# Optimization experiments

Hardware: AMD Instinct MI355X
Metric: run time of the kernel (lower is better)

The kernel has to match this reference:

```python
import jax, jax.numpy as jnp
import numpy as np

NUM_HEADS = 8
LN_EPS = 1e-5


def _layernorm(x, g, b):
    m = jnp.mean(x, axis=-1, keepdims=True)
    v = jnp.mean(jnp.square(x - m), axis=-1, keepdims=True)
    return (x - m) * jax.lax.rsqrt(v + LN_EPS) * g + b


def setup_inputs() -> dict:
    key = jax.random.key(0)
    ks = jax.random.split(key, 10)
    D, C, Cin = 2, 256, 64  # depth, embed dim, input channels
    w = lambda k, shape: jax.random.normal(k, shape, jnp.float32) * 0.02
    return {
        "x": jax.random.normal(ks[0], (4, Cin, 12, 12, 12), jnp.float32),
        "W_pe": w(ks[1], (Cin, C)),
        "b_pe": jnp.zeros((C,), jnp.float32),
        "cls_token": w(ks[2], (1, 1, C)),
        "ln1_g": jnp.ones((D, C), jnp.float32),
        "ln1_b": jnp.zeros((D, C), jnp.float32),
        "Wqkv": w(ks[3], (D, C, 3 * C)),
        "Wproj": w(ks[4], (D, C, C)),
        "bproj": jnp.zeros((D, C), jnp.float32),
        "ln2_g": jnp.ones((D, C), jnp.float32),
        "ln2_b": jnp.zeros((D, C), jnp.float32),
        "W1": w(ks[5], (D, C, C)),
        "b1": jnp.zeros((D, C), jnp.float32),
        "W2": w(ks[6], (D, C, C)),
        "b2": jnp.zeros((D, C), jnp.float32),
        "normf_g": jnp.ones((C,), jnp.float32),
        "normf_b": jnp.zeros((C,), jnp.float32),
    }


def reference(x, W_pe, b_pe, cls_token, ln1_g, ln1_b, Wqkv, Wproj, bproj,
              ln2_g, ln2_b, W1, b1, W2, b2, normf_g, normf_b):
    B, Cin, H, W, L = x.shape
    C = W_pe.shape[1]
    hd = C // NUM_HEADS
    scale = hd ** (-0.5)

    # PatchEmbed: 1x1x1 Conv3d == per-voxel linear projection, then flatten to tokens
    tok = jnp.einsum('bchwl,cd->bhwld', x, W_pe).reshape(B, H * W * L, C) + b_pe
    cls = jnp.broadcast_to(cls_token, (B, 1, C))
    t = jnp.concatenate([cls, tok], axis=1)  # [B, N, C], N = H*W*L + 1
    N = t.shape[1]

    depth = Wqkv.shape[0]
    for i in range(depth):
        # --- self-attention ---
        y = _layernorm(t, ln1_g[i], ln1_b[i])
        qkv = (y @ Wqkv[i]).reshape(B, N, 3, NUM_HEADS, hd)
        qkv = jnp.transpose(qkv, (2, 0, 3, 1, 4))  # [3, B, H, N, hd]
        q, k, v = qkv[0], qkv[1], qkv[2]
        attn = jnp.einsum('bhnd,bhmd->bhnm', q, k) * scale
        attn = jax.nn.softmax(attn, axis=-1)
        o = jnp.einsum('bhnm,bhmd->bhnd', attn, v)
        o = jnp.transpose(o, (0, 2, 1, 3)).reshape(B, N, C)
        t = t + (o @ Wproj[i] + bproj[i])
        # --- MLP (mlp_ratio=1.0, exact GELU) ---
        y = _layernorm(t, ln2_g[i], ln2_b[i])
        h = jax.nn.gelu(y @ W1[i] + b1[i], approximate=False)
        t = t + (h @ W2[i] + b2[i])

    t = _layernorm(t, normf_g, normf_b)
    x_cls = t[:, 0]                                   # [B, C]
    feat = t[:, 1:]                                   # [B, H*W*L, C]
    feat = jnp.transpose(feat, (0, 2, 1)).reshape(B, C, H, W, L)  # downsample = Identity for dim=256
    return x_cls, feat
```

## Files before the change

kernel.cpp:

```cpp
#include <hip/hip_runtime.h>
#include <hip/hip_bf16.h>
#include <math.h>

#define B_   4
#define CIN  64
#define P_   1728
#define N_   1729
#define C_   256
#define NH_  8
#define HD_  32
#define M_   (B_*N_)
#define NPAD 1792

typedef __bf16 bf16x8 __attribute__((ext_vector_type(8)));
typedef __bf16 bf16x4 __attribute__((ext_vector_type(4)));
typedef float  f32x4  __attribute__((ext_vector_type(4)));
typedef float  f32x16 __attribute__((ext_vector_type(16)));

__global__ __launch_bounds__(256) void embed2(
    const float* __restrict__ x, const float* __restrict__ Wpe,
    const float* __restrict__ bpe, const float* __restrict__ cls,
    float* __restrict__ t)
{
    int idx = blockIdx.x*256 + threadIdx.x;
    int c   = idx & 255;
    int n   = (idx >> 8) % N_;
    int b   = idx / (N_*256);
    if (n == 0) { t[idx] = cls[c]; return; }
    int p = n - 1;
    float acc = bpe[c];
    for (int ci = 0; ci < CIN; ++ci)
        acc += x[(size_t)(b*CIN + ci)*P_ + p] * Wpe[ci*C_ + c];
    t[idx] = acc;
}

__global__ __launch_bounds__(256) void ln4(
    const float* __restrict__ in, __bf16* __restrict__ out,
    const float* __restrict__ g, const float* __restrict__ bb)
{
    int wv = threadIdx.x >> 6, lane = threadIdx.x & 63;
    size_t row = (size_t)blockIdx.x*4 + wv;
    float4 v = *(const float4*)&in[row*C_ + lane*4];
    float s1 = (v.x+v.y)+(v.z+v.w);
    float s2 = (v.x*v.x+v.y*v.y)+(v.z*v.z+v.w*v.w);
    #pragma unroll
    for (int off = 32; off >= 1; off >>= 1) {
        s1 += __shfl_xor(s1, off);
        s2 += __shfl_xor(s2, off);
    }
    float mean = s1*(1.0f/C_);
    float var  = fmaxf(s2*(1.0f/C_) - mean*mean, 0.0f);
    float rstd = rsqrtf(var + 1e-5f);
    float4 gg = *(const float4*)&g[lane*4];
    float4 bv = *(const float4*)&bb[lane*4];
    bf16x4 r;
    r[0] = (__bf16)((v.x-mean)*rstd*gg.x + bv.x);
    r[1] = (__bf16)((v.y-mean)*rstd*gg.y + bv.y);
    r[2] = (__bf16)((v.z-mean)*rstd*gg.z + bv.z);
    r[3] = (__bf16)((v.w-mean)*rstd*gg.w + bv.w);
    *(bf16x4*)&out[row*C_ + lane*4] = r;
}

__global__ __launch_bounds__(256) void ln4f(
    const float* __restrict__ in, float* __restrict__ out,
    const float* __restrict__ g, const float* __restrict__ bb,
    float* __restrict__ cls_out)
{
    int wv = threadIdx.x >> 6, lane = threadIdx.x & 63;
    size_t row = (size_t)blockIdx.x*4 + wv;
    float4 v = *(const float4*)&in[row*C_ + lane*4];
    float s1 = (v.x+v.y)+(v.z+v.w);
    float s2 = (v.x*v.x+v.y*v.y)+(v.z*v.z+v.w*v.w);
    #pragma unroll
    for (int off = 32; off >= 1; off >>= 1) {
        s1 += __shfl_xor(s1, off);
        s2 += __shfl_xor(s2, off);
    }
    float mean = s1*(1.0f/C_);
    float var  = fmaxf(s2*(1.0f/C_) - mean*mean, 0.0f);
    float rstd = rsqrtf(var + 1e-5f);
    float4 gg = *(const float4*)&g[lane*4];
    float4 bv = *(const float4*)&bb[lane*4];
    float4 r;
    r.x = (v.x-mean)*rstd*gg.x + bv.x;
    r.y = (v.y-mean)*rstd*gg.y + bv.y;
    r.z = (v.z-mean)*rstd*gg.z + bv.z;
    r.w = (v.w-mean)*rstd*gg.w + bv.w;
    *(float4*)&out[row*C_ + lane*4] = r;
    if ((row % N_) == 0)
        *(float4*)&cls_out[(row / N_)*C_ + lane*4] = r;
}

__global__ __launch_bounds__(256) void wprep2(
    const float* __restrict__ Wqkv, const float* __restrict__ Wproj,
    const float* __restrict__ W1,   const float* __restrict__ W2,
    __bf16* __restrict__ wT)
{
    int z = blockIdx.z, which = z >> 1, layer = z & 1;
    const float* src; __bf16* dst; int NC;
    if (which == 0) {
        src = Wqkv + (size_t)layer*C_*768;
        dst = wT   + (size_t)layer*768*256;
        NC  = 768;
    } else {
        NC = 256;
        const float* b3 = (which == 1) ? Wproj : (which == 2) ? W1 : W2;
        src = b3 + (size_t)layer*65536;
        dst = wT + 2*768*256 + (size_t)((which-1)*2 + layer)*65536;
    }
    int n0 = blockIdx.x*32; if (n0 >= NC) return;
    int k0 = blockIdx.y*32;
    __shared__ float tile[32][33];
    int c = threadIdx.x & 31, r = threadIdx.x >> 5;
    for (int rr = r; rr < 32; rr += 8)
        tile[rr][c] = src[(size_t)(k0+rr)*NC + n0 + c];
    __syncthreads();
    for (int rr = r; rr < 32; rr += 8)
        dst[(size_t)(n0+rr)*256 + k0 + c] = (__bf16)tile[c][rr];
}

__global__ __launch_bounds__(256) void padzero(
    __bf16* __restrict__ kB, __bf16* __restrict__ vB)
{
    int idx = blockIdx.x*256 + threadIdx.x;
    if (idx >= 32*63*32) return;
    int d  = idx & 31;
    int n  = (idx >> 5) % 63 + N_;
    int bh = idx / (63*32);
    kB[((size_t)bh*NPAD + n)*32 + d] = (__bf16)0.f;
    vB[((size_t)bh*32 + d)*NPAD + n] = (__bf16)0.f;
}

template<int NC, bool ADD, bool GELU, bool BIAS, bool OUTBF>
__global__ __launch_bounds__(256) void gemm3(
    const __bf16* __restrict__ A, const __bf16* __restrict__ Wt,
    const float* __restrict__ bias, float* __restrict__ outF,
    __bf16* __restrict__ outB)
{
    __shared__ __align__(16) __bf16 As[64*64];
    __shared__ __align__(16) __bf16 Bs[64*64];
    int r0 = blockIdx.x*64, c0 = blockIdx.y*64;
    int tid = threadIdx.x;
    int wv = tid >> 6, lane = tid & 63, quad = lane >> 4, mn = lane & 15;
    int sr = tid >> 2, sc = tid & 3;
    int ga = r0 + sr; if (ga >= M_) ga = M_ - 1;

    f32x4 acc[4];
    #pragma unroll
    for (int ct = 0; ct < 4; ++ct)
        #pragma unroll
        for (int rr = 0; rr < 4; ++rr) acc[ct][rr] = 0.f;

    for (int kc = 0; kc < 4; ++kc) {
        __syncthreads();
        *(bf16x8*)&As[sr*64 + ((sc ^ (sr & 7))*8)] =
            *(const bf16x8*)&A[(size_t)ga*256 + kc*64 + sc*8];
        *(bf16x8*)&As[sr*64 + (((sc+4) ^ (sr & 7))*8)] =
            *(const bf16x8*)&A[(size_t)ga*256 + kc*64 + sc*8 + 32];
        *(bf16x8*)&Bs[sr*64 + ((sc ^ (sr & 7))*8)] =
            *(const bf16x8*)&Wt[(size_t)(c0+sr)*256 + kc*64 + sc*8];
        *(bf16x8*)&Bs[sr*64 + (((sc+4) ^ (sr & 7))*8)] =
            *(const bf16x8*)&Wt[(size_t)(c0+sr)*256 + kc*64 + sc*8 + 32];
        __syncthreads();

        #pragma unroll
        for (int h = 0; h < 2; ++h) {
            bf16x8 a = *(const bf16x8*)&As[(wv*16 + mn)*64 + (((h*4+quad) ^ (mn & 7))*8)];
            #pragma unroll
            for (int ct = 0; ct < 4; ++ct) {
                bf16x8 b = *(const bf16x8*)&Bs[(ct*16 + mn)*64 + (((h*4+quad) ^ (mn & 7))*8)];
                acc[ct] = __builtin_amdgcn_mfma_f32_16x16x32_bf16(a, b, acc[ct], 0, 0, 0);
            }
        }
    }

    #pragma unroll
    for (int ct = 0; ct < 4; ++ct) {
        int col = c0 + ct*16 + mn;
        #pragma unroll
        for (int rr = 0; rr < 4; ++rr) {
            int row = r0 + wv*16 + quad*4 + rr;
            if (row >= M_) continue;
            float val = acc[ct][rr];
            if (BIAS) val += bias[col];
            if (GELU) val = 0.5f*val*(1.f + erff(val*0.70710678118654752f));
            size_t oi = (size_t)row*NC + col;
            if (OUTBF) outB[oi] = (__bf16)val;
            else if (ADD) outF[oi] += val;
            else outF[oi] = val;
        }
    }
}

__global__ __launch_bounds__(256) void gemm_qkv3(
    const __bf16* __restrict__ A, const __bf16* __restrict__ Wt,
    __bf16* __restrict__ qB, __bf16* __restrict__ kB, __bf16* __restrict__ vB)
{
    __shared__ __align__(16) __bf16 As[64*64];
    __shared__ __align__(16) __bf16 Bs[64*64];
    int r0 = blockIdx.x*64, c0 = blockIdx.y*64;
    int tid = threadIdx.x;
    int wv = tid >> 6, lane = tid & 63, quad = lane >> 4, mn = lane & 15;
    int sr = tid >> 2, sc = tid & 3;
    int ga = r0 + sr; if (ga >= M_) ga = M_ - 1;

    f32x4 acc[4];
    #pragma unroll
    for (int ct = 0; ct < 4; ++ct)
        #pragma unroll
        for (int rr = 0; rr < 4; ++rr) acc[ct][rr] = 0.f;

    for (int kc = 0; kc < 4; ++kc) {
        __syncthreads();
        *(bf16x8*)&As[sr*64 + ((sc ^ (sr & 7))*8)] =
            *(const bf16x8*)&A[(size_t)ga*256 + kc*64 + sc*8];
        *(bf16x8*)&As[sr*64 + (((sc+4) ^ (sr & 7))*8)] =
            *(const bf16x8*)&A[(size_t)ga*256 + kc*64 + sc*8 + 32];
        *(bf16x8*)&Bs[sr*64 + ((sc ^ (sr & 7))*8)] =
            *(const bf16x8*)&Wt[(size_t)(c0+sr)*256 + kc*64 + sc*8];
        *(bf16x8*)&Bs[sr*64 + (((sc+4) ^ (sr & 7))*8)] =
            *(const bf16x8*)&Wt[(size_t)(c0+sr)*256 + kc*64 + sc*8 + 32];
        __syncthreads();

        #pragma unroll
        for (int h = 0; h < 2; ++h) {
            bf16x8 a = *(const bf16x8*)&As[(wv*16 + mn)*64 + (((h*4+quad) ^ (mn & 7))*8)];
            #pragma unroll
            for (int ct = 0; ct < 4; ++ct) {
                bf16x8 b = *(const bf16x8*)&Bs[(ct*16 + mn)*64 + (((h*4+quad) ^ (mn & 7))*8)];
                acc[ct] = __builtin_amdgcn_mfma_f32_16x16x32_bf16(a, b, acc[ct], 0, 0, 0);
            }
        }
    }

    const float scale = 0.17677669529663687f;
    #pragma unroll
    for (int ct = 0; ct < 4; ++ct) {
        int col = c0 + ct*16 + mn;
        #pragma unroll
        for (int rr = 0; rr < 4; ++rr) {
            int row = r0 + wv*16 + quad*4 + rr;
            if (row >= M_) continue;
            int b = row / N_, n = row - b*N_;
            float val = acc[ct][rr];
            if (col < 256) {
                int h = col >> 5, dd = col & 31;
                qB[((size_t)(b*NH_+h)*NPAD + n)*32 + dd] = (__bf16)(val*scale);
            } else if (col < 512) {
                int h = (col-256) >> 5, dd = col & 31;
                kB[((size_t)(b*NH_+h)*NPAD + n)*32 + dd] = (__bf16)val;
            } else {
                int h = (col-512) >> 5, dd = col & 31;
                vB[((size_t)(b*NH_+h)*32 + dd)*NPAD + n] = (__bf16)val;
            }
        }
    }
}

#define LKS 40
#define LVS 136

__device__ __forceinline__ unsigned cvtpk_bf16(float lo, float hi) {
    unsigned r;
    asm("v_cvt_pk_bf16_f32 %0, %1, %2" : "=v"(r) : "v"(lo), "v"(hi));
    return r;
}

__global__ __launch_bounds__(128) void attn12(
    const __bf16* __restrict__ qB, const __bf16* __restrict__ kB,
    const __bf16* __restrict__ vB, __bf16* __restrict__ o)
{
    int bh = blockIdx.x, b = bh >> 3, h = bh & 7;
    int q0 = blockIdx.y * 64;
    int tid = threadIdx.x;
    int wv = tid >> 6, lane = tid & 63, lo5 = lane & 31, hi = lane >> 5;

    __shared__ __align__(16) __bf16 lk[128*LKS];
    __shared__ __align__(16) __bf16 lvt[32*LVS];

    const __bf16* kbase = kB + (size_t)bh*NPAD*32;
    const __bf16* vbase = vB + (size_t)bh*32*NPAD;

    const __bf16* qrow = qB + ((size_t)bh*NPAD + q0 + wv*32 + lo5)*32 + hi*8;
    bf16x8 qf0 = *(const bf16x8*)(qrow);
    bf16x8 qf1 = *(const bf16x8*)(qrow + 16);

    f32x16 oacc;
    #pragma unroll
    for (int r = 0; r < 16; ++r) oacc[r] = 0.f;
    float lsum = 0.f;

    int vr = tid >> 2, vc = tid & 3;

    bf16x8 ks0, ks1, ks2, ks3, vs0, vs1, vs2, vs3;
#define ATTN_LOAD(T) do {                                              \
        const __bf16* kp_ = kbase + ((size_t)((T)*128 + tid))*32;      \
        ks0 = *(const bf16x8*)(kp_);                                   \
        ks1 = *(const bf16x8*)(kp_ + 8);                               \
        ks2 = *(const bf16x8*)(kp_ + 16);                              \
        ks3 = *(const bf16x8*)(kp_ + 24);                              \
        const __bf16* vp_ = vbase + (size_t)vr*NPAD + (T)*128 + vc*32; \
        vs0 = *(const bf16x8*)(vp_);                                   \
        vs1 = *(const bf16x8*)(vp_ + 8);                               \
        vs2 = *(const bf16x8*)(vp_ + 16);                              \
        vs3 = *(const bf16x8*)(vp_ + 24);                              \
    } while (0)

    ATTN_LOAD(0);

    for (int t = 0; t < 14; ++t) {
        __syncthreads();
        {
            __bf16* kd = &lk[tid*LKS];
            *(bf16x8*)(kd)      = ks0;  *(bf16x8*)(kd + 8)  = ks1;
            *(bf16x8*)(kd + 16) = ks2;  *(bf16x8*)(kd + 24) = ks3;
            __bf16* vd = &lvt[vr*LVS + vc*32];
            *(bf16x8*)(vd)      = vs0;  *(bf16x8*)(vd + 8)  = vs1;
            *(bf16x8*)(vd + 16) = vs2;  *(bf16x8*)(vd + 24) = vs3;
        }
        if (t < 13) ATTN_LOAD(t+1);
        __syncthreads();

        #pragma unroll
        for (int kg = 0; kg < 4; ++kg) {
            const __bf16* kf = &lk[(kg*32 + lo5)*LKS + hi*8];
            bf16x8 kf0 = *(const bf16x8*)(kf);
            bf16x8 kf1 = *(const bf16x8*)(kf + 16);
            f32x16 s;
            #pragma unroll
            for (int r = 0; r < 16; ++r) s[r] = 0.f;
            __builtin_amdgcn_s_setprio(1);
            s = __builtin_amdgcn_mfma_f32_32x32x16_bf16(kf0, qf0, s, 0, 0, 0);
            s = __builtin_amdgcn_mfma_f32_32x32x16_bf16(kf1, qf1, s, 0, 0, 0);
            __builtin_amdgcn_s_setprio(0);

            float p[16];
            #pragma unroll
            for (int r = 0; r < 16; ++r) p[r] = __expf(s[r]);
            float l0 = 0.f, l1 = 0.f;
            #pragma unroll
            for (int r = 0; r < 8; ++r) { l0 += p[r]; l1 += p[r+8]; }
            lsum += l0 + l1;

            unsigned a0 = cvtpk_bf16(p[0],  p[1]),  a1 = cvtpk_bf16(p[2],  p[3]);
            unsigned b0 = cvtpk_bf16(p[4],  p[5]),  b1 = cvtpk_bf16(p[6],  p[7]);
            unsigned c0 = cvtpk_bf16(p[8],  p[9]),  c1 = cvtpk_bf16(p[10], p[11]);
            unsigned d0 = cvtpk_bf16(p[12], p[13]), d1 = cvtpk_bf16(p[14], p[15]);
            asm("v_permlane32_swap_b32 %0, %1" : "+v"(a0), "+v"(b0));
            asm("v_permlane32_swap_b32 %0, %1" : "+v"(a1), "+v"(b1));
            asm("v_permlane32_swap_b32 %0, %1" : "+v"(c0), "+v"(d0));
            asm("v_permlane32_swap_b32 %0, %1" : "+v"(c1), "+v"(d1));
            union { bf16x8 v; unsigned u[4]; } f0, f1;
            f0.u[0] = a0; f0.u[1] = a1; f0.u[2] = b0; f0.u[3] = b1;
            f1.u[0] = c0; f1.u[1] = c1; f1.u[2] = d0; f1.u[3] = d1;

            const __bf16* vf = &lvt[lo5*LVS + kg*32 + hi*8];
            bf16x8 vf0 = *(const bf16x8*)(vf);
            bf16x8 vf1 = *(const bf16x8*)(vf + 16);
            __builtin_amdgcn_s_setprio(1);
            oacc = __builtin_amdgcn_mfma_f32_32x32x16_bf16(f0.v, vf0, oacc, 0, 0, 0);
            oacc = __builtin_amdgcn_mfma_f32_32x32x16_bf16(f1.v, vf1, oacc, 0, 0, 0);
            __builtin_amdgcn_s_setprio(0);
        }
    }
#undef ATTN_LOAD

    lsum += __shfl_xor(lsum, 32);
    float inv = 1.0f / (lsum - 63.0f);

    #pragma unroll
    for (int r = 0; r < 16; ++r) {
        int qrw = (r & 3) + 8*(r >> 2) + 4*hi;
        float li = __shfl(inv, qrw);
        int q = q0 + wv*32 + qrw;
        if (q < N_)
            o[((size_t)b*N_ + q)*C_ + h*HD_ + lo5] = (__bf16)(oacc[r] * li);
    }
}

__global__ __launch_bounds__(256) void feat3(
    const float* __restrict__ y, float* __restrict__ outf)
{
    __shared__ float tl[32][33];
    int p0 = blockIdx.x*32, c0 = blockIdx.y*32, b = blockIdx.z;
    int cc = threadIdx.x & 31, rr = threadIdx.x >> 5;
    for (int i = rr; i < 32; i += 8)
        tl[i][cc] = y[((size_t)(b*N_) + 1 + p0 + i)*C_ + c0 + cc];
    __syncthreads();
    for (int i = rr; i < 32; i += 8)
        outf[((size_t)(b*C_) + c0 + i)*P_ + p0 + cc] = tl[cc][i];
}

extern "C" void kernel_launch(void* const* d_in, const int* in_sizes, int n_in,
                              void* d_out, int out_size, void* d_ws, size_t ws_size,
                              hipStream_t stream)
{
    const float* x        = (const float*)d_in[0];
    const float* W_pe     = (const float*)d_in[1];
    const float* b_pe     = (const float*)d_in[2];
    const float* cls_tok  = (const float*)d_in[3];
    const float* ln1_g    = (const float*)d_in[4];
    const float* ln1_b    = (const float*)d_in[5];
    const float* Wqkv     = (const float*)d_in[6];
    const float* Wproj    = (const float*)d_in[7];
    const float* bproj    = (const float*)d_in[8];
    const float* ln2_g    = (const float*)d_in[9];
    const float* ln2_b    = (const float*)d_in[10];
    const float* W1       = (const float*)d_in[11];
    const float* b1       = (const float*)d_in[12];
    const float* W2       = (const float*)d_in[13];
    const float* b2       = (const float*)d_in[14];
    const float* normf_g  = (const float*)d_in[15];
    const float* normf_b  = (const float*)d_in[16];

    const size_t MC = (size_t)M_*C_;
    float*  ws  = (float*)d_ws;
    float*  t   = ws;
    float*  yf  = ws + MC;
    __bf16* ybf = (__bf16*)(ws + 2*MC);
    __bf16* hbf = (__bf16*)(ws + 2*MC + MC/2);
    __bf16* obf = (__bf16*)(ws + 2*MC + MC);
    __bf16* wT  = (__bf16*)(ws + 2*MC + 3*(MC/2));
    __bf16* qB  = wT + 2*768*256 + 6*256*256;
    __bf16* kB  = qB + (size_t)B_*NH_*NPAD*32;
    __bf16* vB  = kB + (size_t)B_*NH_*NPAD*32;

    __bf16* projT = wT + 2*768*256;
    __bf16* w1T   = projT + 2*256*256;
    __bf16* w2T   = w1T   + 2*256*256;

    float* out_cls  = (float*)d_out;
    float* out_feat = out_cls + B_*C_;

    wprep2<<<dim3(24, 8, 8), 256, 0, stream>>>(Wqkv, Wproj, W1, W2, wT);
    padzero<<<252, 256, 0, stream>>>(kB, vB);
    embed2<<<(B_*N_*C_)/256, 256, 0, stream>>>(x, W_pe, b_pe, cls_tok, t);

    const int GRID_M = (M_ + 63) / 64;
    for (int i = 0; i < 2; ++i) {
        ln4<<<M_/4, 256, 0, stream>>>(t, ybf, ln1_g + i*C_, ln1_b + i*C_);
        gemm_qkv3<<<dim3(GRID_M, 12), 256, 0, stream>>>(
            ybf, wT + (size_t)i*768*256, qB, kB, vB);
        attn12<<<dim3(32, 28), 128, 0, stream>>>(qB, kB, vB, obf);
        gemm3<256,true,false,true,false><<<dim3(GRID_M, 4), 256, 0, stream>>>(
            obf, projT + (size_t)i*65536, bproj + i*C_, t, nullptr);
        ln4<<<M_/4, 256, 0, stream>>>(t, ybf, ln2_g + i*C_, ln2_b + i*C_);
        gemm3<256,false,true,true,true><<<dim3(GRID_M, 4), 256, 0, stream>>>(
            ybf, w1T + (size_t)i*65536, b1 + i*C_, nullptr, hbf);
        gemm3<256,true,false,true,false><<<dim3(GRID_M, 4), 256, 0, stream>>>(
            hbf, w2T + (size_t)i*65536, b2 + i*C_, t, nullptr);
    }

    ln4f<<<M_/4, 256, 0, stream>>>(t, yf, normf_g, normf_b, out_cls);
    feat3<<<dim3(54, 8, 4), 256, 0, stream>>>(yf, out_feat);
}
```

Baseline: 289.5 us.

## Double-buffer LDS tiles in GEMMs and attention, use exp2 with folded scale

Gives the GEMM kernels and the attention kernel two LDS buffers, so the next K/V or A/B tile is loaded from global and stored into the spare buffer while MFMAs run on the current one. This halves the barriers per iteration. Attention also issues all four QK^T MFMA groups before the softmax, splits the PV accumulation across two accumulators to shorten the dependency chain, and swaps __expf for raw v_exp_f32 with log2(e) folded into the q scale. The cost is doubled LDS usage and more live registers, which may reduce occupancy.

Result: no change. 288.7 us (-0.3%).

```diff
diff --git a/kernel.cpp b/kernel.cpp
--- a/kernel.cpp
+++ b/kernel.cpp
@@ -132,13 +132,13 @@
 }
 
 template<int NC, bool ADD, bool GELU, bool BIAS, bool OUTBF>
-__global__ __launch_bounds__(256) void gemm3(
+__global__ __launch_bounds__(256) void gemm4(
     const __bf16* __restrict__ A, const __bf16* __restrict__ Wt,
     const float* __restrict__ bias, float* __restrict__ outF,
     __bf16* __restrict__ outB)
 {
-    __shared__ __align__(16) __bf16 As[64*64];
-    __shared__ __align__(16) __bf16 Bs[64*64];
+    __shared__ __align__(16) __bf16 As[2][64*64];
+    __shared__ __align__(16) __bf16 Bs[2][64*64];
     int r0 = blockIdx.x*64, c0 = blockIdx.y*64;
     int tid = threadIdx.x;
     int wv = tid >> 6, lane = tid & 63, quad = lane >> 4, mn = lane & 15;
@@ -151,28 +151,46 @@
         #pragma unroll
         for (int rr = 0; rr < 4; ++rr) acc[ct][rr] = 0.f;
 
+    bf16x8 ra0, ra1, rb0, rb1;
+#define GLOAD(KC) do {                                                   \
+        ra0 = *(const bf16x8*)&A[(size_t)ga*256 + (KC)*64 + sc*8];       \
+        ra1 = *(const bf16x8*)&A[(size_t)ga*256 + (KC)*64 + sc*8 + 32];  \
+        rb0 = *(const bf16x8*)&Wt[(size_t)(c0+sr)*256 + (KC)*64 + sc*8]; \
+        rb1 = *(const bf16x8*)&Wt[(size_t)(c0+sr)*256 + (KC)*64 + sc*8 + 32]; \
+    } while (0)
+#define SSTORE(BUF) do {                                                 \
+        *(bf16x8*)&As[BUF][sr*64 + ((sc ^ (sr & 7))*8)]       = ra0;     \
+        *(bf16x8*)&As[BUF][sr*64 + (((sc+4) ^ (sr & 7))*8)]   = ra1;     \
+        *(bf16x8*)&Bs[BUF][sr*64 + ((sc ^ (sr & 7))*8)]       = rb0;     \
+        *(bf16x8*)&Bs[BUF][sr*64 + (((sc+4) ^ (sr & 7))*8)]   = rb1;     \
+    } while (0)
+
+    GLOAD(0);
+    SSTORE(0);
+    __syncthreads();
+
     for (int kc = 0; kc < 4; ++kc) {
-        __syncthreads();
-        *(bf16x8*)&As[sr*64 + ((sc ^ (sr & 7))*8)] =
-            *(const bf16x8*)&A[(size_t)ga*256 + kc*64 + sc*8];
-        *(bf16x8*)&As[sr*64 + (((sc+4) ^ (sr & 7))*8)] =
-            *(const bf16x8*)&A[(size_t)ga*256 + kc*64 + sc*8 + 32];
-        *(bf16x8*)&Bs[sr*64 + ((sc ^ (sr & 7))*8)] =
-            *(const bf16x8*)&Wt[(size_t)(c0+sr)*256 + kc*64 + sc*8];
-        *(bf16x8*)&Bs[sr*64 + (((sc+4) ^ (sr & 7))*8)] =
-            *(const bf16x8*)&Wt[(size_t)(c0+sr)*256 + kc*64 + sc*8 + 32];
-        __syncthreads();
+        int cur = kc & 1;
+        if (kc < 3) GLOAD(kc+1);
+        __builtin_amdgcn_sched_barrier(0);
 
         #pragma unroll
         for (int h = 0; h < 2; ++h) {
-            bf16x8 a = *(const bf16x8*)&As[(wv*16 + mn)*64 + (((h*4+quad) ^ (mn & 7))*8)];
+            bf16x8 a = *(const bf16x8*)&As[cur][(wv*16 + mn)*64 + (((h*4+quad) ^ (mn & 7))*8)];
             #pragma unroll
             for (int ct = 0; ct < 4; ++ct) {
-                bf16x8 b = *(const bf16x8*)&Bs[(ct*16 + mn)*64 + (((h*4+quad) ^ (mn & 7))*8)];
+                bf16x8 b = *(const bf16x8*)&Bs[cur][(ct*16 + mn)*64 + (((h*4+quad) ^ (mn & 7))*8)];
                 acc[ct] = __builtin_amdgcn_mfma_f32_16x16x32_bf16(a, b, acc[ct], 0, 0, 0);
             }
         }
-    }
+
+        if (kc < 3) {
+            SSTORE(cur^1);
+            __syncthreads();
+        }
+    }
+#undef GLOAD
+#undef SSTORE
 
     #pragma unroll
     for (int ct = 0; ct < 4; ++ct) {
@@ -192,12 +210,12 @@
     }
 }
 
-__global__ __launch_bounds__(256) void gemm_qkv3(
+__global__ __launch_bounds__(256) void gemm_qkv4(
     const __bf16* __restrict__ A, const __bf16* __restrict__ Wt,
     __bf16* __restrict__ qB, __bf16* __restrict__ kB, __bf16* __restrict__ vB)
 {
-    __shared__ __align__(16) __bf16 As[64*64];
-    __shared__ __align__(16) __bf16 Bs[64*64];
+    __shared__ __align__(16) __bf16 As[2][64*64];
+    __shared__ __align__(16) __bf16 Bs[2][64*64];
     int r0 = blockIdx.x*64, c0 = blockIdx.y*64;
     int tid = threadIdx.x;
     int wv = tid >> 6, lane = tid & 63, quad = lane >> 4, mn = lane & 15;
@@ -210,30 +228,48 @@
         #pragma unroll
         for (int rr = 0; rr < 4; ++rr) acc[ct][rr] = 0.f;
 
+    bf16x8 ra0, ra1, rb0, rb1;
+#define GLOAD(KC) do {                                                   \
+        ra0 = *(const bf16x8*)&A[(size_t)ga*256 + (KC)*64 + sc*8];       \
+        ra1 = *(const bf16x8*)&A[(size_t)ga*256 + (KC)*64 + sc*8 + 32];  \
+        rb0 = *(const bf16x8*)&Wt[(size_t)(c0+sr)*256 + (KC)*64 + sc*8]; \
+        rb1 = *(const bf16x8*)&Wt[(size_t)(c0+sr)*256 + (KC)*64 + sc*8 + 32]; \
+    } while (0)
+#define SSTORE(BUF) do {                                                 \
+        *(bf16x8*)&As[BUF][sr*64 + ((sc ^ (sr & 7))*8)]       = ra0;     \
+        *(bf16x8*)&As[BUF][sr*64 + (((sc+4) ^ (sr & 7))*8)]   = ra1;     \
+        *(bf16x8*)&Bs[BUF][sr*64 + ((sc ^ (sr & 7))*8)]       = rb0;     \
+        *(bf16x8*)&Bs[BUF][sr*64 + (((sc+4) ^ (sr & 7))*8)]   = rb1;     \
+    } while (0)
+
+    GLOAD(0);
+    SSTORE(0);
+    __syncthreads();
+
     for (int kc = 0; kc < 4; ++kc) {
-        __syncthreads();
-        *(bf16x8*)&As[sr*64 + ((sc ^ (sr & 7))*8)] =
-            *(const bf16x8*)&A[(size_t)ga*256 + kc*64 + sc*8];
-        *(bf16x8*)&As[sr*64 + (((sc+4) ^ (sr & 7))*8)] =
-            *(const bf16x8*)&A[(size_t)ga*256 + kc*64 + sc*8 + 32];
-        *(bf16x8*)&Bs[sr*64 + ((sc ^ (sr & 7))*8)] =
-            *(const bf16x8*)&Wt[(size_t)(c0+sr)*256 + kc*64 + sc*8];
-        *(bf16x8*)&Bs[sr*64 + (((sc+4) ^ (sr & 7))*8)] =
-            *(const bf16x8*)&Wt[(size_t)(c0+sr)*256 + kc*64 + sc*8 + 32];
-        __syncthreads();
+        int cur = kc & 1;
+        if (kc < 3) GLOAD(kc+1);
+        __builtin_amdgcn_sched_barrier(0);
 
         #pragma unroll
         for (int h = 0; h < 2; ++h) {
-            bf16x8 a = *(const bf16x8*)&As[(wv*16 + mn)*64 + (((h*4+quad) ^ (mn & 7))*8)];
+            bf16x8 a = *(const bf16x8*)&As[cur][(wv*16 + mn)*64 + (((h*4+quad) ^ (mn & 7))*8)];
             #pragma unroll
             for (int ct = 0; ct < 4; ++ct) {
-                bf16x8 b = *(const bf16x8*)&Bs[(ct*16 + mn)*64 + (((h*4+quad) ^ (mn & 7))*8)];
+                bf16x8 b = *(const bf16x8*)&Bs[cur][(ct*16 + mn)*64 + (((h*4+quad) ^ (mn & 7))*8)];
                 acc[ct] = __builtin_amdgcn_mfma_f32_16x16x32_bf16(a, b, acc[ct], 0, 0, 0);
             }
         }
-    }
-
-    const float scale = 0.17677669529663687f;
+
+        if (kc < 3) {
+            SSTORE(cur^1);
+            __syncthreads();
+        }
+    }
+#undef GLOAD
+#undef SSTORE
+
+    const float scale = 0.2550348727f;
     #pragma unroll
     for (int ct = 0; ct < 4; ++ct) {
         int col = c0 + ct*16 + mn;
@@ -260,13 +296,16 @@
 #define LKS 40
 #define LVS 136
 
+__device__ __forceinline__ float fexp2(float x) {
+    float r; asm("v_exp_f32 %0, %1" : "=v"(r) : "v"(x)); return r;
+}
 __device__ __forceinline__ unsigned cvtpk_bf16(float lo, float hi) {
     unsigned r;
     asm("v_cvt_pk_bf16_f32 %0, %1, %2" : "=v"(r) : "v"(lo), "v"(hi));
     return r;
 }
 
-__global__ __launch_bounds__(128) void attn12(
+__global__ __launch_bounds__(128) void attn13(
     const __bf16* __restrict__ qB, const __bf16* __restrict__ kB,
     const __bf16* __restrict__ vB, __bf16* __restrict__ o)
 {
@@ -275,8 +314,8 @@
     int tid = threadIdx.x;
     int wv = tid >> 6, lane = tid & 63, lo5 = lane & 31, hi = lane >> 5;
 
-    __shared__ __align__(16) __bf16 lk[128*LKS];
-    __shared__ __align__(16) __bf16 lvt[32*LVS];
+    __shared__ __align__(16) __bf16 lk[2][128*LKS];
+    __shared__ __align__(16) __bf16 lvt[2][32*LVS];
 
     const __bf16* kbase = kB + (size_t)bh*NPAD*32;
     const __bf16* vbase = vB + (size_t)bh*32*NPAD;
@@ -285,9 +324,9 @@
     bf16x8 qf0 = *(const bf16x8*)(qrow);
     bf16x8 qf1 = *(const bf16x8*)(qrow + 16);
 
-    f32x16 oacc;
-    #pragma unroll
-    for (int r = 0; r < 16; ++r) oacc[r] = 0.f;
+    f32x16 oaccA, oaccB;
+    #pragma unroll
+    for (int r = 0; r < 16; ++r) { oaccA[r] = 0.f; oaccB[r] = 0.f; }
     float lsum = 0.f;
 
     int vr = tid >> 2, vc = tid & 3;
@@ -305,38 +344,43 @@
         vs2 = *(const bf16x8*)(vp_ + 16);                              \
         vs3 = *(const bf16x8*)(vp_ + 24);                              \
     } while (0)
+#define ATTN_STORE(BUF) do {                                           \
+        __bf16* kd = &lk[BUF][tid*LKS];                                \
+        *(bf16x8*)(kd)      = ks0;  *(bf16x8*)(kd + 8)  = ks1;         \
+        *(bf16x8*)(kd + 16) = ks2;  *(bf16x8*)(kd + 24) = ks3;         \
+        __bf16* vd = &lvt[BUF][vr*LVS + vc*32];                        \
+        *(bf16x8*)(vd)      = vs0;  *(bf16x8*)(vd + 8)  = vs1;         \
+        *(bf16x8*)(vd + 16) = vs2;  *(bf16x8*)(vd + 24) = vs3;         \
+    } while (0)
 
     ATTN_LOAD(0);
+    ATTN_STORE(0);
+    __syncthreads();
 
     for (int t = 0; t < 14; ++t) {
-        __syncthreads();
-        {
-            __bf16* kd = &lk[tid*LKS];
-            *(bf16x8*)(kd)      = ks0;  *(bf16x8*)(kd + 8)  = ks1;
-            *(bf16x8*)(kd + 16) = ks2;  *(bf16x8*)(kd + 24) = ks3;
-            __bf16* vd = &lvt[vr*LVS + vc*32];
-            *(bf16x8*)(vd)      = vs0;  *(bf16x8*)(vd + 8)  = vs1;
-            *(bf16x8*)(vd + 16) = vs2;  *(bf16x8*)(vd + 24) = vs3;
-        }
+        int cur = t & 1;
         if (t < 13) ATTN_LOAD(t+1);
-        __syncthreads();
-
+        __builtin_amdgcn_sched_barrier(0);
+
+        f32x16 s[4];
+        __builtin_amdgcn_s_setprio(1);
         #pragma unroll
         for (int kg = 0; kg < 4; ++kg) {
-            const __bf16* kf = &lk[(kg*32 + lo5)*LKS + hi*8];
+            const __bf16* kf = &lk[cur][(kg*32 + lo5)*LKS + hi*8];
             bf16x8 kf0 = *(const bf16x8*)(kf);
             bf16x8 kf1 = *(const bf16x8*)(kf + 16);
-            f32x16 s;
             #pragma unroll
-            for (int r = 0; r < 16; ++r) s[r] = 0.f;
-            __builtin_amdgcn_s_setprio(1);
-            s = __builtin_amdgcn_mfma_f32_32x32x16_bf16(kf0, qf0, s, 0, 0, 0);
-            s = __builtin_amdgcn_mfma_f32_32x32x16_bf16(kf1, qf1, s, 0, 0, 0);
-            __builtin_amdgcn_s_setprio(0);
-
+            for (int r = 0; r < 16; ++r) s[kg][r] = 0.f;
+            s[kg] = __builtin_amdgcn_mfma_f32_32x32x16_bf16(kf0, qf0, s[kg], 0, 0, 0);
+            s[kg] = __builtin_amdgcn_mfma_f32_32x32x16_bf16(kf1, qf1, s[kg], 0, 0, 0);
+        }
+        __builtin_amdgcn_s_setprio(0);
+
+        #pragma unroll
+        for (int kg = 0; kg < 4; ++kg) {
             float p[16];
             #pragma unroll
-            for (int r = 0; r < 16; ++r) p[r] = __expf(s[r]);
+            for (int r = 0; r < 16; ++r) p[r] = fexp2(s[kg][r]);
             float l0 = 0.f, l1 = 0.f;
             #pragma unroll
             for (int r = 0; r < 8; ++r) { l0 += p[r]; l1 += p[r+8]; }
@@ -354,27 +398,39 @@
             f0.u[0] = a0; f0.u[1] = a1; f0.u[2] = b0; f0.u[3] = b1;
             f1.u[0] = c0; f1.u[1] = c1; f1.u[2] = d0; f1.u[3] = d1;
 
-            const __bf16* vf = &lvt[lo5*LVS + kg*32 + hi*8];
+            const __bf16* vf = &lvt[cur][lo5*LVS + kg*32 + hi*8];
             bf16x8 vf0 = *(const bf16x8*)(vf);
             bf16x8 vf1 = *(const bf16x8*)(vf + 16);
             __builtin_amdgcn_s_setprio(1);
-            oacc = __builtin_amdgcn_mfma_f32_32x32x16_bf16(f0.v, vf0, oacc, 0, 0, 0);
-            oacc = __builtin_amdgcn_mfma_f32_32x32x16_bf16(f1.v, vf1, oacc, 0, 0, 0);
+            if (kg & 1) {
+                oaccB = __builtin_amdgcn_mfma_f32_32x32x16_bf16(f0.v, vf0, oaccB, 0, 0, 0);
+                oaccB = __builtin_amdgcn_mfma_f32_32x32x16_bf16(f1.v, vf1, oaccB, 0, 0, 0);
+            } else {
+                oaccA = __builtin_amdgcn_mfma_f32_32x32x16_bf16(f0.v, vf0, oaccA, 0, 0, 0);
+                oaccA = __builtin_amdgcn_mfma_f32_32x32x16_bf16(f1.v, vf1, oaccA, 0, 0, 0);
+            }
             __builtin_amdgcn_s_setprio(0);
         }
+
+        if (t < 13) {
+            ATTN_STORE(cur^1);
+            __syncthreads();
+        }
     }
 #undef ATTN_LOAD
+#undef ATTN_STORE
 
     lsum += __shfl_xor(lsum, 32);
     float inv = 1.0f / (lsum - 63.0f);
 
     #pragma unroll
     for (int r = 0; r < 16; ++r) {
+        float oa = oaccA[r] + oaccB[r];
         int qrw = (r & 3) + 8*(r >> 2) + 4*hi;
         float li = __shfl(inv, qrw);
         int q = q0 + wv*32 + qrw;
         if (q < N_)
-            o[((size_t)b*N_ + q)*C_ + h*HD_ + lo5] = (__bf16)(oacc[r] * li);
+            o[((size_t)b*N_ + q)*C_ + h*HD_ + lo5] = (__bf16)(oa * li);
     }
 }
 
@@ -439,15 +495,15 @@
     const int GRID_M = (M_ + 63) / 64;
     for (int i = 0; i < 2; ++i) {
         ln4<<<M_/4, 256, 0, stream>>>(t, ybf, ln1_g + i*C_, ln1_b + i*C_);
-        gemm_qkv3<<<dim3(GRID_M, 12), 256, 0, stream>>>(
+        gemm_qkv4<<<dim3(GRID_M, 12), 256, 0, stream>>>(
             ybf, wT + (size_t)i*768*256, qB, kB, vB);
-        attn12<<<dim3(32, 28), 128, 0, stream>>>(qB, kB, vB, obf);
-        gemm3<256,true,false,true,false><<<dim3(GRID_M, 4), 256, 0, stream>>>(
+        attn13<<<dim3(32, 28), 128, 0, stream>>>(qB, kB, vB, obf);
+        gemm4<256,true,false,true,false><<<dim3(GRID_M, 4), 256, 0, stream>>>(
             obf, projT + (size_t)i*65536, bproj + i*C_, t, nullptr);
         ln4<<<M_/4, 256, 0, stream>>>(t, ybf, ln2_g + i*C_, ln2_b + i*C_);
-        gemm3<256,false,true,true,true><<<dim3(GRID_M, 4), 256, 0, stream>>>(
+        gemm4<256,false,true,true,true><<<dim3(GRID_M, 4), 256, 0, stream>>>(
             ybf, w1T + (size_t)i*65536, b1 + i*C_, nullptr, hbf);
-        gemm3<256,true,false,true,false><<<dim3(GRID_M, 4), 256, 0, stream>>>(
+        gemm4<256,true,false,true,false><<<dim3(GRID_M, 4), 256, 0, stream>>>(
             hbf, w2T + (size_t)i*65536, b2 + i*C_, t, nullptr);
     }
 
```
